# Performance work log

Hardware: AMD Instinct MI355X
Metric: run time of the kernel (lower is better)

Reference implementation:

```python
import jax, jax.numpy as jnp
import numpy as np

WS = (2, 6, 12)          # window_size (Z, H, W)
DIM = 192
HEADS = 6
TOW = 240                # type_of_windows = (8//2)*(360//6)
NW = 720                 # total number of windows = 3 * TOW
L = WS[0] * WS[1] * WS[2]  # 144 tokens per window


def _position_index(ws):
    """Replicates EarthAttention3D._construct_index (static int index)."""
    zi = np.arange(ws[0]); zj = -np.arange(ws[0]) * ws[0]
    hi = np.arange(ws[1]); hj = -np.arange(ws[1]) * ws[1]
    w = np.arange(ws[2])
    c1 = np.stack(np.meshgrid(zi, hi, w, indexing='ij')).reshape(3, -1)
    c2 = np.stack(np.meshgrid(zj, hj, w, indexing='ij')).reshape(3, -1)
    coords = (c1[:, :, None] - c2[:, None, :]).transpose(1, 2, 0)  # (L, L, 3)
    coords[:, :, 2] += ws[2] - 1
    coords[:, :, 1] *= 2 * ws[2] - 1
    coords[:, :, 0] *= (2 * ws[2] - 1) * ws[1] * ws[1]
    return coords.sum(-1).reshape(-1)  # (L*L,)

POS_INDEX = jnp.asarray(_position_index(WS))


def setup_inputs() -> dict:
    key = jax.random.key(0)
    ks = jax.random.split(key, 4)
    table_len = (2 * WS[2] - 1) * WS[1] * WS[1] * WS[0] * WS[0]  # 3312
    return {
        "x": jax.random.normal(ks[0], (NW, L, DIM), jnp.float32),
        "mask": jnp.zeros((NW, L, L), jnp.float32),
        "w1": jax.random.normal(ks[1], (3 * DIM, DIM), jnp.float32) * 0.02,
        "b1": jnp.zeros((3 * DIM,), jnp.float32),
        "w2": jax.random.normal(ks[2], (DIM, DIM), jnp.float32) * 0.02,
        "b2": jnp.zeros((DIM,), jnp.float32),
        "bias_table": jax.random.normal(ks[3], (table_len, TOW, HEADS), jnp.float32) * 0.02,
    }


def reference(x, mask, w1, b1, w2, b2, bias_table):
    Wn, Ltok, dim = x.shape
    hd = dim // HEADS
    scale = hd ** -0.5
    # qkv projection: (Wn, L, 3, H, hd) -> q,k,v each (Wn, H, L, hd)
    qkv = (x @ w1.T + b1).reshape(Wn, Ltok, 3, HEADS, hd)
    qkv = jnp.transpose(qkv, (2, 0, 3, 1, 4))
    q, k, v = qkv[0], qkv[1], qkv[2]
    attn = jnp.einsum('whid,whjd->whij', q * scale, k)  # (Wn, H, L, L)
    # Earth-specific bias: gather table -> (L, L, TOW, H) -> (TOW, H, L, L)
    bias = bias_table[POS_INDEX].reshape(Ltok, Ltok, TOW, HEADS)
    bias = jnp.transpose(bias, (2, 3, 0, 1))
    # tile across window axis exactly like the concat loop, then slice
    reps = Wn // TOW + 1
    bias = jnp.tile(bias, (reps, 1, 1, 1))[:Wn][None]  # (1, Wn, H, L, L)
    attn = attn[None] + bias                            # (1, Wn, H, L, L)
    attn = attn + mask[None, :, None, :, :]             # mask.unsqueeze(1).unsqueeze(0)
    attn = jax.nn.softmax(attn, axis=-1)
    out = jnp.einsum('bwhij,whjd->bwhid', attn, v)      # (1, Wn, H, L, hd)
    out = jnp.transpose(out, (0, 1, 3, 2, 4)).reshape(Wn, Ltok, dim)
    out = out @ w2.T + b2
    return out
```

## Files before the change

kernel.cpp:

```cpp
#include <hip/hip_runtime.h>
#include <cstdint>
#include <cstddef>


using short8 = __attribute__((ext_vector_type(8))) short;
using f32x4  = __attribute__((ext_vector_type(4))) float;

constexpr int kNW = 720;
constexpr float kScale = 0.17677669529663687f;
constexpr size_t kQKVElems = (size_t)kNW * 6 * 144 * 32;

__device__ __forceinline__ ushort bf16_rne(float f) {
  uint u = __builtin_bit_cast(uint, f);
  return (ushort)((u + 0x7FFFu + ((u >> 16) & 1u)) >> 16);
}
__device__ __forceinline__ float bf16_to_f(ushort h) {
  uint u = ((uint)h) << 16;
  return __builtin_bit_cast(float, u);
}
__device__ __forceinline__ uint pack_hl(float f) {
  const ushort h = bf16_rne(f);
  const ushort l = bf16_rne(f - bf16_to_f(h));
  return ((uint)h << 16) | l;
}

__global__ __launch_bounds__(256) void prep_kernel(
    const float* __restrict__ src, ushort* __restrict__ dh,
    ushort* __restrict__ dl, int n)
{
  const int i = blockIdx.x * 256 + threadIdx.x;
  if (i < n) {
    const float f = src[i];
    const ushort h = bf16_rne(f);
    dh[i] = h;
    dl[i] = bf16_rne(f - bf16_to_f(h));
  }
}

__global__ __launch_bounds__(256) void btT_kernel(
    const float* __restrict__ bt, float* __restrict__ btT)
{
  __shared__ float T[48][49];
  const int pb = (blockIdx.x % 69) * 48;
  const int bb = (blockIdx.x / 69) * 48;
  const int tid = threadIdx.x;
  for (int f = tid; f < 2304; f += 256) {
    const int r = f / 48, c = f % 48;
    T[r][c] = bt[(size_t)(pb + r) * 1440 + bb + c];
  }
  __syncthreads();
  for (int f = tid; f < 2304; f += 256) {
    const int r = f % 48, c = f / 48;
    btT[(size_t)(bb + c) * 3312 + pb + r] = T[r][c];
  }
}

template <bool IS_QKV>
__global__ __launch_bounds__(512) void gemm_kernel(
    const float* __restrict__ Xf, const uint* __restrict__ Xp,
    const ushort* __restrict__ Wh, const ushort* __restrict__ Wl,
    const float* __restrict__ bias,
    uint* __restrict__ qp, uint* __restrict__ kp, uint* __restrict__ vp,
    float* __restrict__ fout)
{
  __shared__ ushort Ah[128][40], Al[128][40];
  __shared__ ushort Bh[192][40], Bl[192][40];

  const int bid = blockIdx.x;
  const int mtile = IS_QKV ? bid / 3 : bid;
  const int col0  = IS_QKV ? (bid % 3) * 192 : 0;
  const int row0 = mtile * 128;
  const int tid = threadIdx.x;
  const int wave = tid >> 6, lane = tid & 63;
  const int rr = lane & 15, kg = lane >> 4;
  const int wm = wave >> 2, wn = wave & 3;

  f32x4 acc[4][3];
#pragma unroll
  for (int a = 0; a < 4; ++a)
#pragma unroll
    for (int b = 0; b < 3; ++b) acc[a][b] = (f32x4){0.f, 0.f, 0.f, 0.f};

  for (int kc = 0; kc < 192; kc += 32) {
#pragma unroll
    for (int u = 0; u < 2; ++u) {
      const int sl = tid + u * 512;
      const int r = sl >> 3, s = sl & 7;
      if constexpr (IS_QKV) {
        float4 xv = *(const float4*)&Xf[(size_t)(row0 + r) * 192 + kc + s * 4];
        ushort4 hv, lv;
        hv.x = bf16_rne(xv.x); lv.x = bf16_rne(xv.x - bf16_to_f(hv.x));
        hv.y = bf16_rne(xv.y); lv.y = bf16_rne(xv.y - bf16_to_f(hv.y));
        hv.z = bf16_rne(xv.z); lv.z = bf16_rne(xv.z - bf16_to_f(hv.z));
        hv.w = bf16_rne(xv.w); lv.w = bf16_rne(xv.w - bf16_to_f(hv.w));
        *(ushort4*)&Ah[r][s * 4] = hv;
        *(ushort4*)&Al[r][s * 4] = lv;
      } else {
        uint4 a = *(const uint4*)&Xp[(size_t)(row0 + r) * 192 + kc + s * 4];
        uint2 hh, ll;
        hh.x = (a.x >> 16) | (a.y & 0xffff0000u);
        hh.y = (a.z >> 16) | (a.w & 0xffff0000u);
        ll.x = (a.x & 0xffffu) | (a.y << 16);
        ll.y = (a.z & 0xffffu) | (a.w << 16);
        *(uint2*)&Ah[r][s * 4] = hh;
        *(uint2*)&Al[r][s * 4] = ll;
      }
    }
#pragma unroll
    for (int u = 0; u < 3; ++u) {
      const int idx = tid + u * 512;
      const int n = idx >> 3, s2 = idx & 7;
      const size_t g = (size_t)(col0 + n) * 192 + kc + s2 * 4;
      *(uint2*)&Bh[n][s2 * 4] = *(const uint2*)&Wh[g];
      *(uint2*)&Bl[n][s2 * 4] = *(const uint2*)&Wl[g];
    }
    __syncthreads();

    short8 ah[4], al_[4], bh[3], bl[3];
#pragma unroll
    for (int mt = 0; mt < 4; ++mt) {
      const int r = wm * 64 + mt * 16 + rr;
      ah[mt]  = *(const short8*)&Ah[r][kg * 8];
      al_[mt] = *(const short8*)&Al[r][kg * 8];
    }
#pragma unroll
    for (int nt = 0; nt < 3; ++nt) {
      const int n = wn * 48 + nt * 16 + rr;
      bh[nt] = *(const short8*)&Bh[n][kg * 8];
      bl[nt] = *(const short8*)&Bl[n][kg * 8];
    }
#pragma unroll
    for (int mt = 0; mt < 4; ++mt)
#pragma unroll
      for (int nt = 0; nt < 3; ++nt) {
        acc[mt][nt] = __builtin_amdgcn_mfma_f32_16x16x32_bf16(ah[mt],  bh[nt], acc[mt][nt], 0, 0, 0);
        acc[mt][nt] = __builtin_amdgcn_mfma_f32_16x16x32_bf16(ah[mt],  bl[nt], acc[mt][nt], 0, 0, 0);
        acc[mt][nt] = __builtin_amdgcn_mfma_f32_16x16x32_bf16(al_[mt], bh[nt], acc[mt][nt], 0, 0, 0);
      }
    __syncthreads();
  }

  if (IS_QKV) {
    const int t = col0 / 192;
    uint* dst = (t == 0) ? qp : (t == 1) ? kp : vp;
    const float sc = (t == 0) ? kScale : 1.0f;
#pragma unroll
    for (int nt = 0; nt < 3; ++nt) {
      const int c0 = wn * 48 + nt * 16;
      const int hh = c0 >> 5;
      const int d0 = (c0 & 31) + rr;
      const float bcol = bias[col0 + c0 + rr];
#pragma unroll
      for (int mt = 0; mt < 4; ++mt)
#pragma unroll
        for (int reg = 0; reg < 4; ++reg) {
          const int grow = row0 + wm * 64 + mt * 16 + kg * 4 + reg;
          const int w = grow / 144;
          const int l = grow % 144;
          dst[(((size_t)(w * 6 + hh)) * 144 + l) * 32 + d0] =
              pack_hl((acc[mt][nt][reg] + bcol) * sc);
        }
    }
  } else {
#pragma unroll
    for (int nt = 0; nt < 3; ++nt) {
      const int c = wn * 48 + nt * 16 + rr;
      const float bcol = bias[c];
#pragma unroll
      for (int mt = 0; mt < 4; ++mt)
#pragma unroll
        for (int reg = 0; reg < 4; ++reg) {
          const int grow = row0 + wm * 64 + mt * 16 + kg * 4 + reg;
          fout[(size_t)grow * 192 + c] = acc[mt][nt][reg] + bcol;
        }
    }
  }
}

__device__ __forceinline__ void attn_unit(
    const ushort (&KsH)[144][40], const ushort (&KsL)[144][40],
    const ushort (&VtH)[32][168], const ushort (&VtL)[32][168],
    uint* __restrict__ scrw,
    const uint* __restrict__ qpb, const float* __restrict__ mrow,
    const float* __restrict__ brow, uint* __restrict__ aopb,
    int wave, int rr, int kg)
{
  const int i0 = wave * 16;
  const int i = i0 + rr;
  const int pi = 828 * (i / 72) + 23 * ((i / 12) % 6) + (i % 12) + 11;

  const uint4 qa = *(const uint4*)&qpb[(size_t)i * 32 + kg * 8];
  const uint4 qb = *(const uint4*)&qpb[(size_t)i * 32 + kg * 8 + 4];
  float4 mv[9], bv[9];
#pragma unroll
  for (int jt = 0; jt < 9; ++jt) {
    const int jb = jt * 16 + kg * 4;
    mv[jt] = *(const float4*)&mrow[(size_t)i * 144 + jb];
    const int pjb = 1656 * (jb / 72) + 138 * ((jb / 12) % 6) - (jb % 12);
    bv[jt] = *(const float4*)&brow[pi + pjb - 3];
  }

  union { short8 v; uint u[4]; } QH, QL;
  QH.u[0] = (qa.x >> 16) | (qa.y & 0xffff0000u);
  QH.u[1] = (qa.z >> 16) | (qa.w & 0xffff0000u);
  QH.u[2] = (qb.x >> 16) | (qb.y & 0xffff0000u);
  QH.u[3] = (qb.z >> 16) | (qb.w & 0xffff0000u);
  QL.u[0] = (qa.x & 0xffffu) | (qa.y << 16);
  QL.u[1] = (qa.z & 0xffffu) | (qa.w << 16);
  QL.u[2] = (qb.x & 0xffffu) | (qb.y << 16);
  QL.u[3] = (qb.z & 0xffffu) | (qb.w << 16);

  f32x4 acc[9];
#pragma unroll
  for (int jt = 0; jt < 9; ++jt) {
    const short8 kah = *(const short8*)&KsH[jt * 16 + rr][kg * 8];
    const short8 kal = *(const short8*)&KsL[jt * 16 + rr][kg * 8];
    f32x4 c = (f32x4){0.f, 0.f, 0.f, 0.f};
    c = __builtin_amdgcn_mfma_f32_16x16x32_bf16(kah, QH.v, c, 0, 0, 0);
    c = __builtin_amdgcn_mfma_f32_16x16x32_bf16(kah, QL.v, c, 0, 0, 0);
    c = __builtin_amdgcn_mfma_f32_16x16x32_bf16(kal, QH.v, c, 0, 0, 0);
    c[0] += bv[jt].w + mv[jt].x;
    c[1] += bv[jt].z + mv[jt].y;
    c[2] += bv[jt].y + mv[jt].z;
    c[3] += bv[jt].x + mv[jt].w;
    acc[jt] = c;
  }

  float m = -1e30f;
#pragma unroll
  for (int jt = 0; jt < 9; ++jt)
    m = fmaxf(m, fmaxf(fmaxf(acc[jt][0], acc[jt][1]),
                       fmaxf(acc[jt][2], acc[jt][3])));
  m = fmaxf(m, __shfl_xor(m, 16));
  m = fmaxf(m, __shfl_xor(m, 32));
  float s = 0.f;
#pragma unroll
  for (int jt = 0; jt < 9; ++jt)
#pragma unroll
    for (int r = 0; r < 4; ++r) {
      acc[jt][r] = __expf(acc[jt][r] - m);
      s += acc[jt][r];
    }
  s += __shfl_xor(s, 16);
  s += __shfl_xor(s, 32);
  const float inv = 1.0f / s;

  uint wh_[10][2], wl_[10][2];
#pragma unroll
  for (int jt = 0; jt < 9; ++jt)
#pragma unroll
    for (int u = 0; u < 2; ++u) {
      const float p0 = acc[jt][2 * u] * inv, p1 = acc[jt][2 * u + 1] * inv;
      const ushort h0 = bf16_rne(p0), h1 = bf16_rne(p1);
      const ushort l0 = bf16_rne(p0 - bf16_to_f(h0));
      const ushort l1 = bf16_rne(p1 - bf16_to_f(h1));
      wh_[jt][u] = (uint)h0 | ((uint)h1 << 16);
      wl_[jt][u] = (uint)l0 | ((uint)l1 << 16);
    }
  wh_[9][0] = 0; wh_[9][1] = 0; wl_[9][0] = 0; wl_[9][1] = 0;

  f32x4 oacc[2] = {(f32x4){0.f, 0.f, 0.f, 0.f}, (f32x4){0.f, 0.f, 0.f, 0.f}};
#pragma unroll
  for (int ks = 0; ks < 5; ++ks) {
    const int jtA = 2 * ks, jtB = 2 * ks + 1;
    *(uint2*)&scrw[rr * 20 + 2 * kg]           = make_uint2(wh_[jtA][0], wh_[jtA][1]);
    *(uint2*)&scrw[rr * 20 + 8 + 2 * kg]       = make_uint2(wh_[jtB][0], wh_[jtB][1]);
    *(uint2*)&scrw[320 + rr * 20 + 2 * kg]     = make_uint2(wl_[jtA][0], wl_[jtA][1]);
    *(uint2*)&scrw[320 + rr * 20 + 8 + 2 * kg] = make_uint2(wl_[jtB][0], wl_[jtB][1]);
    asm volatile("s_waitcnt lgkmcnt(0)" ::: "memory");
    const ushort* scr = (const ushort*)scrw;
    const short8 pfh = *(const short8*)&scr[rr * 40 + kg * 8];
    const short8 pfl = *(const short8*)&scr[640 + rr * 40 + kg * 8];
#pragma unroll
    for (int dt = 0; dt < 2; ++dt) {
      const short8 vfh = *(const short8*)&VtH[dt * 16 + rr][ks * 32 + kg * 8];
      const short8 vfl = *(const short8*)&VtL[dt * 16 + rr][ks * 32 + kg * 8];
      oacc[dt] = __builtin_amdgcn_mfma_f32_16x16x32_bf16(pfh, vfh, oacc[dt], 0, 0, 0);
      oacc[dt] = __builtin_amdgcn_mfma_f32_16x16x32_bf16(pfh, vfl, oacc[dt], 0, 0, 0);
      oacc[dt] = __builtin_amdgcn_mfma_f32_16x16x32_bf16(pfl, vfh, oacc[dt], 0, 0, 0);
    }
    asm volatile("s_waitcnt lgkmcnt(0)" ::: "memory");
  }

#pragma unroll
  for (int dt = 0; dt < 2; ++dt)
#pragma unroll
    for (int r = 0; r < 4; ++r)
      aopb[(size_t)(i0 + kg * 4 + r) * 192 + dt * 16 + rr] =
          pack_hl(oacc[dt][r]);
}

__device__ __forceinline__ void write_k(
    ushort (&KH)[144][40], ushort (&KL)[144][40], int l, int d, uint4 kv)
{
  ushort4 hk, lk;
  hk.x = (ushort)(kv.x >> 16); lk.x = (ushort)(kv.x & 0xffff);
  hk.y = (ushort)(kv.y >> 16); lk.y = (ushort)(kv.y & 0xffff);
  hk.z = (ushort)(kv.z >> 16); lk.z = (ushort)(kv.z & 0xffff);
  hk.w = (ushort)(kv.w >> 16); lk.w = (ushort)(kv.w & 0xffff);
  *(ushort4*)&KH[l][d] = hk;
  *(ushort4*)&KL[l][d] = lk;
}
__device__ __forceinline__ void write_vt(
    ushort (&VH)[32][168], ushort (&VL)[32][168], int l, int d, uint4 vv)
{
  VH[d + 0][l] = (ushort)(vv.x >> 16); VL[d + 0][l] = (ushort)(vv.x & 0xffff);
  VH[d + 1][l] = (ushort)(vv.y >> 16); VL[d + 1][l] = (ushort)(vv.y & 0xffff);
  VH[d + 2][l] = (ushort)(vv.z >> 16); VL[d + 2][l] = (ushort)(vv.z & 0xffff);
  VH[d + 3][l] = (ushort)(vv.w >> 16); VL[d + 3][l] = (ushort)(vv.w & 0xffff);
}

__global__ __launch_bounds__(576) void attn_kernel(
    const uint* __restrict__ qp, const uint* __restrict__ kp,
    const uint* __restrict__ vp, const float* __restrict__ mask,
    const float* __restrict__ btT, uint* __restrict__ aop)
{
  __shared__ __align__(16) ushort Ks_[3][2][144][40];
  __shared__ __align__(16) ushort Vt[3][2][32][168];
  __shared__ __align__(16) uint Scr[9][640];

  const int tid = threadIdx.x;
  const int wave = tid >> 6, lane = tid & 63;
  const int rr = lane & 15, kg = lane >> 4;

  const int b = blockIdx.x;
  const int q = (b & 7) * 180 + (b >> 3);
  const int w = q >> 1;
  const int h0 = (q & 1) * 3;
  const size_t base0 = (size_t)(w * 6 + h0) * 4608;
  const float* mrow = mask + (size_t)w * 20736;
  const float* brow0 = btT + (size_t)((w % 240) * 6 + h0) * 3312;
  uint* aopb0 = aop + (size_t)w * 144 * 192 + h0 * 32;

  const int l0 = tid >> 3, d0 = (tid & 7) * 4;
  const int f1 = tid + 576;
  const int l1 = f1 >> 3, d1 = (f1 & 7) * 4;

  {
    const uint4 kvA = *(const uint4*)&kp[base0 + l0 * 32 + d0];
    const uint4 vvA = *(const uint4*)&vp[base0 + l0 * 32 + d0];
    const uint4 kvB = *(const uint4*)&kp[base0 + l1 * 32 + d1];
    const uint4 vvB = *(const uint4*)&vp[base0 + l1 * 32 + d1];
    write_k(Ks_[0][0], Ks_[0][1], l0, d0, kvA);
    write_k(Ks_[0][0], Ks_[0][1], l1, d1, kvB);
    write_vt(Vt[0][0], Vt[0][1], l0, d0, vvA);
    write_vt(Vt[0][0], Vt[0][1], l1, d1, vvB);
  }
  for (int f = tid; f < 3072; f += 576) {
    const int bu = f >> 10, pl = (f >> 9) & 1, d = (f >> 4) & 31, j = 144 + (f & 15);
    Vt[bu][pl][d][j] = 0;
  }

  uint4 kA = *(const uint4*)&kp[base0 + 4608 + l0 * 32 + d0];
  uint4 vA = *(const uint4*)&vp[base0 + 4608 + l0 * 32 + d0];
  uint4 kB = *(const uint4*)&kp[base0 + 4608 + l1 * 32 + d1];
  uint4 vB = *(const uint4*)&vp[base0 + 4608 + l1 * 32 + d1];

  __syncthreads();

  attn_unit(Ks_[0][0], Ks_[0][1], Vt[0][0], Vt[0][1], Scr[wave],
            qp + base0, mrow, brow0, aopb0, wave, rr, kg);

  write_k(Ks_[1][0], Ks_[1][1], l0, d0, kA);
  write_k(Ks_[1][0], Ks_[1][1], l1, d1, kB);
  write_vt(Vt[1][0], Vt[1][1], l0, d0, vA);
  write_vt(Vt[1][0], Vt[1][1], l1, d1, vB);
  kA = *(const uint4*)&kp[base0 + 9216 + l0 * 32 + d0];
  vA = *(const uint4*)&vp[base0 + 9216 + l0 * 32 + d0];
  kB = *(const uint4*)&kp[base0 + 9216 + l1 * 32 + d1];
  vB = *(const uint4*)&vp[base0 + 9216 + l1 * 32 + d1];

  __syncthreads();

  attn_unit(Ks_[1][0], Ks_[1][1], Vt[1][0], Vt[1][1], Scr[wave],
            qp + base0 + 4608, mrow, brow0 + 3312, aopb0 + 32, wave, rr, kg);

  write_k(Ks_[2][0], Ks_[2][1], l0, d0, kA);
  write_k(Ks_[2][0], Ks_[2][1], l1, d1, kB);
  write_vt(Vt[2][0], Vt[2][1], l0, d0, vA);
  write_vt(Vt[2][0], Vt[2][1], l1, d1, vB);

  __syncthreads();

  attn_unit(Ks_[2][0], Ks_[2][1], Vt[2][0], Vt[2][1], Scr[wave],
            qp + base0 + 9216, mrow, brow0 + 6624, aopb0 + 64, wave, rr, kg);
}

extern "C" void kernel_launch(void* const* d_in, const int* in_sizes, int n_in,
                              void* d_out, int out_size, void* d_ws, size_t ws_size,
                              hipStream_t stream)
{
  const float* x    = (const float*)d_in[0];
  const float* mask = (const float*)d_in[1];
  const float* w1   = (const float*)d_in[2];
  const float* b1   = (const float*)d_in[3];
  const float* w2   = (const float*)d_in[4];
  const float* b2   = (const float*)d_in[5];
  const float* bt   = (const float*)d_in[6];
  float* out = (float*)d_out;

  uint* qp  = (uint*)d_ws;
  uint* kp  = qp + kQKVElems;
  uint* vp  = kp + kQKVElems;
  uint* aop = vp + kQKVElems;
  ushort* w1h = (ushort*)aop;
  ushort* w1l = w1h + 110592;
  ushort* w2h = (ushort*)qp;
  ushort* w2l = w2h + 36864;
  float* btT = out;

  btT_kernel<<<69 * 30, 256, 0, stream>>>(bt, btT);
  prep_kernel<<<432, 256, 0, stream>>>(w1, w1h, w1l, 110592);
  gemm_kernel<true><<<810 * 3, 512, 0, stream>>>(
      x, nullptr, w1h, w1l, b1, qp, kp, vp, nullptr);
  attn_kernel<<<1440, 576, 0, stream>>>(qp, kp, vp, mask, btT, aop);
  prep_kernel<<<144, 256, 0, stream>>>(w2, w2h, w2l, 36864);
  gemm_kernel<false><<<810, 512, 0, stream>>>(
      nullptr, aop, w2h, w2l, b2, nullptr, nullptr, nullptr, out);
}
```

Before: 358.7 us.

## Fuse output projection into attention kernel, one block per window over six heads

The output projection GEMM is folded into the attention kernel. Each block now handles all six heads of a window, double-buffers K/V through shared memory, and accumulates the per-head attention output times the matching W2 slice in registers. This removes the intermediate attention-output buffer round trip and a separate kernel launch. In exchange the grid is halved to 720 blocks, each wave keeps 12 extra accumulators, W2 fragments are read from global memory per head, and the bias table moves into workspace instead of reusing the output buffer.

```diff
diff --git a/kernel.cpp b/kernel.cpp
--- a/kernel.cpp
+++ b/kernel.cpp
@@ -55,20 +55,18 @@
   }
 }
 
-template <bool IS_QKV>
-__global__ __launch_bounds__(512) void gemm_kernel(
-    const float* __restrict__ Xf, const uint* __restrict__ Xp,
+__global__ __launch_bounds__(512) void qkv_gemm_kernel(
+    const float* __restrict__ Xf,
     const ushort* __restrict__ Wh, const ushort* __restrict__ Wl,
     const float* __restrict__ bias,
-    uint* __restrict__ qp, uint* __restrict__ kp, uint* __restrict__ vp,
-    float* __restrict__ fout)
+    uint* __restrict__ qp, uint* __restrict__ kp, uint* __restrict__ vp)
 {
   __shared__ ushort Ah[128][40], Al[128][40];
   __shared__ ushort Bh[192][40], Bl[192][40];
 
   const int bid = blockIdx.x;
-  const int mtile = IS_QKV ? bid / 3 : bid;
-  const int col0  = IS_QKV ? (bid % 3) * 192 : 0;
+  const int mtile = bid / 3;
+  const int col0  = (bid % 3) * 192;
   const int row0 = mtile * 128;
   const int tid = threadIdx.x;
   const int wave = tid >> 6, lane = tid & 63;
@@ -86,25 +84,14 @@
     for (int u = 0; u < 2; ++u) {
       const int sl = tid + u * 512;
       const int r = sl >> 3, s = sl & 7;
-      if constexpr (IS_QKV) {
-        float4 xv = *(const float4*)&Xf[(size_t)(row0 + r) * 192 + kc + s * 4];
-        ushort4 hv, lv;
-        hv.x = bf16_rne(xv.x); lv.x = bf16_rne(xv.x - bf16_to_f(hv.x));
-        hv.y = bf16_rne(xv.y); lv.y = bf16_rne(xv.y - bf16_to_f(hv.y));
-        hv.z = bf16_rne(xv.z); lv.z = bf16_rne(xv.z - bf16_to_f(hv.z));
-        hv.w = bf16_rne(xv.w); lv.w = bf16_rne(xv.w - bf16_to_f(hv.w));
-        *(ushort4*)&Ah[r][s * 4] = hv;
-        *(ushort4*)&Al[r][s * 4] = lv;
-      } else {
-        uint4 a = *(const uint4*)&Xp[(size_t)(row0 + r) * 192 + kc + s * 4];
-        uint2 hh, ll;
-        hh.x = (a.x >> 16) | (a.y & 0xffff0000u);
-        hh.y = (a.z >> 16) | (a.w & 0xffff0000u);
-        ll.x = (a.x & 0xffffu) | (a.y << 16);
-        ll.y = (a.z & 0xffffu) | (a.w << 16);
-        *(uint2*)&Ah[r][s * 4] = hh;
-        *(uint2*)&Al[r][s * 4] = ll;
-      }
+      float4 xv = *(const float4*)&Xf[(size_t)(row0 + r) * 192 + kc + s * 4];
+      ushort4 hv, lv;
+      hv.x = bf16_rne(xv.x); lv.x = bf16_rne(xv.x - bf16_to_f(hv.x));
+      hv.y = bf16_rne(xv.y); lv.y = bf16_rne(xv.y - bf16_to_f(hv.y));
+      hv.z = bf16_rne(xv.z); lv.z = bf16_rne(xv.z - bf16_to_f(hv.z));
+      hv.w = bf16_rne(xv.w); lv.w = bf16_rne(xv.w - bf16_to_f(hv.w));
+      *(ushort4*)&Ah[r][s * 4] = hv;
+      *(ushort4*)&Al[r][s * 4] = lv;
     }
 #pragma unroll
     for (int u = 0; u < 3; ++u) {
@@ -140,50 +127,36 @@
     __syncthreads();
   }
 
-  if (IS_QKV) {
-    const int t = col0 / 192;
-    uint* dst = (t == 0) ? qp : (t == 1) ? kp : vp;
-    const float sc = (t == 0) ? kScale : 1.0f;
-#pragma unroll
-    for (int nt = 0; nt < 3; ++nt) {
-      const int c0 = wn * 48 + nt * 16;
-      const int hh = c0 >> 5;
-      const int d0 = (c0 & 31) + rr;
-      const float bcol = bias[col0 + c0 + rr];
-#pragma unroll
-      for (int mt = 0; mt < 4; ++mt)
-#pragma unroll
-        for (int reg = 0; reg < 4; ++reg) {
-          const int grow = row0 + wm * 64 + mt * 16 + kg * 4 + reg;
-          const int w = grow / 144;
-          const int l = grow % 144;
-          dst[(((size_t)(w * 6 + hh)) * 144 + l) * 32 + d0] =
-              pack_hl((acc[mt][nt][reg] + bcol) * sc);
-        }
-    }
-  } else {
-#pragma unroll
-    for (int nt = 0; nt < 3; ++nt) {
-      const int c = wn * 48 + nt * 16 + rr;
-      const float bcol = bias[c];
-#pragma unroll
-      for (int mt = 0; mt < 4; ++mt)
-#pragma unroll
-        for (int reg = 0; reg < 4; ++reg) {
-          const int grow = row0 + wm * 64 + mt * 16 + kg * 4 + reg;
-          fout[(size_t)grow * 192 + c] = acc[mt][nt][reg] + bcol;
-        }
-    }
-  }
-}
-
-__device__ __forceinline__ void attn_unit(
+  const int t = col0 / 192;
+  uint* dst = (t == 0) ? qp : (t == 1) ? kp : vp;
+  const float sc = (t == 0) ? kScale : 1.0f;
+#pragma unroll
+  for (int nt = 0; nt < 3; ++nt) {
+    const int c0 = wn * 48 + nt * 16;
+    const int hh = c0 >> 5;
+    const int d0 = (c0 & 31) + rr;
+    const float bcol = bias[col0 + c0 + rr];
+#pragma unroll
+    for (int mt = 0; mt < 4; ++mt)
+#pragma unroll
+      for (int reg = 0; reg < 4; ++reg) {
+        const int grow = row0 + wm * 64 + mt * 16 + kg * 4 + reg;
+        const int w = grow / 144;
+        const int l = grow % 144;
+        dst[(((size_t)(w * 6 + hh)) * 144 + l) * 32 + d0] =
+            pack_hl((acc[mt][nt][reg] + bcol) * sc);
+      }
+  }
+}
+
+__device__ __forceinline__ void attn_unit_fused(
     const ushort (&KsH)[144][40], const ushort (&KsL)[144][40],
     const ushort (&VtH)[32][168], const ushort (&VtL)[32][168],
     uint* __restrict__ scrw,
     const uint* __restrict__ qpb, const float* __restrict__ mrow,
-    const float* __restrict__ brow, uint* __restrict__ aopb,
-    int wave, int rr, int kg)
+    const float* __restrict__ brow,
+    const ushort* __restrict__ w2h, const ushort* __restrict__ w2l,
+    int u, f32x4* pacc, int wave, int rr, int kg)
 {
   const int i0 = wave * 16;
   const int i = i0 + rr;
@@ -200,15 +173,15 @@
     bv[jt] = *(const float4*)&brow[pi + pjb - 3];
   }
 
-  union { short8 v; uint u[4]; } QH, QL;
-  QH.u[0] = (qa.x >> 16) | (qa.y & 0xffff0000u);
-  QH.u[1] = (qa.z >> 16) | (qa.w & 0xffff0000u);
-  QH.u[2] = (qb.x >> 16) | (qb.y & 0xffff0000u);
-  QH.u[3] = (qb.z >> 16) | (qb.w & 0xffff0000u);
-  QL.u[0] = (qa.x & 0xffffu) | (qa.y << 16);
-  QL.u[1] = (qa.z & 0xffffu) | (qa.w << 16);
-  QL.u[2] = (qb.x & 0xffffu) | (qb.y << 16);
-  QL.u[3] = (qb.z & 0xffffu) | (qb.w << 16);
+  union { short8 v; uint uu[4]; } QH, QL;
+  QH.uu[0] = (qa.x >> 16) | (qa.y & 0xffff0000u);
+  QH.uu[1] = (qa.z >> 16) | (qa.w & 0xffff0000u);
+  QH.uu[2] = (qb.x >> 16) | (qb.y & 0xffff0000u);
+  QH.uu[3] = (qb.z >> 16) | (qb.w & 0xffff0000u);
+  QL.uu[0] = (qa.x & 0xffffu) | (qa.y << 16);
+  QL.uu[1] = (qa.z & 0xffffu) | (qa.w << 16);
+  QL.uu[2] = (qb.x & 0xffffu) | (qb.y << 16);
+  QL.uu[3] = (qb.z & 0xffffu) | (qb.w << 16);
 
   f32x4 acc[9];
 #pragma unroll
@@ -249,13 +222,13 @@
 #pragma unroll
   for (int jt = 0; jt < 9; ++jt)
 #pragma unroll
-    for (int u = 0; u < 2; ++u) {
-      const float p0 = acc[jt][2 * u] * inv, p1 = acc[jt][2 * u + 1] * inv;
+    for (int uu = 0; uu < 2; ++uu) {
+      const float p0 = acc[jt][2 * uu] * inv, p1 = acc[jt][2 * uu + 1] * inv;
       const ushort h0 = bf16_rne(p0), h1 = bf16_rne(p1);
       const ushort l0 = bf16_rne(p0 - bf16_to_f(h0));
       const ushort l1 = bf16_rne(p1 - bf16_to_f(h1));
-      wh_[jt][u] = (uint)h0 | ((uint)h1 << 16);
-      wl_[jt][u] = (uint)l0 | ((uint)l1 << 16);
+      wh_[jt][uu] = (uint)h0 | ((uint)h1 << 16);
+      wl_[jt][uu] = (uint)l0 | ((uint)l1 << 16);
     }
   wh_[9][0] = 0; wh_[9][1] = 0; wl_[9][0] = 0; wl_[9][1] = 0;
 
@@ -282,12 +255,33 @@
     asm volatile("s_waitcnt lgkmcnt(0)" ::: "memory");
   }
 
-#pragma unroll
-  for (int dt = 0; dt < 2; ++dt)
-#pragma unroll
-    for (int r = 0; r < 4; ++r)
-      aopb[(size_t)(i0 + kg * 4 + r) * 192 + dt * 16 + rr] =
-          pack_hl(oacc[dt][r]);
+  {
+    ushort* sh = (ushort*)scrw;
+#pragma unroll
+    for (int dt = 0; dt < 2; ++dt)
+#pragma unroll
+      for (int r = 0; r < 4; ++r) {
+        const int il = kg * 4 + r;
+        const int dl = dt * 16 + rr;
+        const float v = oacc[dt][r];
+        const ushort h = bf16_rne(v);
+        sh[il * 40 + dl] = h;
+        sh[640 + il * 40 + dl] = bf16_rne(v - bf16_to_f(h));
+      }
+    asm volatile("s_waitcnt lgkmcnt(0)" ::: "memory");
+    const short8 pah = *(const short8*)&sh[rr * 40 + kg * 8];
+    const short8 pal = *(const short8*)&sh[640 + rr * 40 + kg * 8];
+#pragma unroll
+    for (int nt = 0; nt < 12; ++nt) {
+      const size_t gb = (size_t)(nt * 16 + rr) * 192 + u * 32 + kg * 8;
+      const short8 wbh = *(const short8*)&w2h[gb];
+      const short8 wbl = *(const short8*)&w2l[gb];
+      pacc[nt] = __builtin_amdgcn_mfma_f32_16x16x32_bf16(pah, wbh, pacc[nt], 0, 0, 0);
+      pacc[nt] = __builtin_amdgcn_mfma_f32_16x16x32_bf16(pah, wbl, pacc[nt], 0, 0, 0);
+      pacc[nt] = __builtin_amdgcn_mfma_f32_16x16x32_bf16(pal, wbh, pacc[nt], 0, 0, 0);
+    }
+    asm volatile("s_waitcnt lgkmcnt(0)" ::: "memory");
+  }
 }
 
 __device__ __forceinline__ void write_k(
@@ -313,10 +307,12 @@
 __global__ __launch_bounds__(576) void attn_kernel(
     const uint* __restrict__ qp, const uint* __restrict__ kp,
     const uint* __restrict__ vp, const float* __restrict__ mask,
-    const float* __restrict__ btT, uint* __restrict__ aop)
-{
-  __shared__ __align__(16) ushort Ks_[3][2][144][40];
-  __shared__ __align__(16) ushort Vt[3][2][32][168];
+    const float* __restrict__ btT,
+    const ushort* __restrict__ w2h, const ushort* __restrict__ w2l,
+    const float* __restrict__ b2, float* __restrict__ out)
+{
+  __shared__ __align__(16) ushort Ks_[2][2][144][40];
+  __shared__ __align__(16) ushort Vt[2][2][32][168];
   __shared__ __align__(16) uint Scr[9][640];
 
   const int tid = threadIdx.x;
@@ -324,13 +320,11 @@
   const int rr = lane & 15, kg = lane >> 4;
 
   const int b = blockIdx.x;
-  const int q = (b & 7) * 180 + (b >> 3);
-  const int w = q >> 1;
-  const int h0 = (q & 1) * 3;
-  const size_t base0 = (size_t)(w * 6 + h0) * 4608;
+  const int w = (b & 7) * 90 + (b >> 3);
+  const size_t base0 = (size_t)(w * 6) * 4608;
   const float* mrow = mask + (size_t)w * 20736;
-  const float* brow0 = btT + (size_t)((w % 240) * 6 + h0) * 3312;
-  uint* aopb0 = aop + (size_t)w * 144 * 192 + h0 * 32;
+  const float* brow0 = btT + (size_t)((w % 240) * 6) * 3312;
+  float* out_b = out + (size_t)w * 144 * 192;
 
   const int l0 = tid >> 3, d0 = (tid & 7) * 4;
   const int f1 = tid + 576;
@@ -346,10 +340,14 @@
     write_vt(Vt[0][0], Vt[0][1], l0, d0, vvA);
     write_vt(Vt[0][0], Vt[0][1], l1, d1, vvB);
   }
-  for (int f = tid; f < 3072; f += 576) {
+  for (int f = tid; f < 2048; f += 576) {
     const int bu = f >> 10, pl = (f >> 9) & 1, d = (f >> 4) & 31, j = 144 + (f & 15);
     Vt[bu][pl][d][j] = 0;
   }
+
+  f32x4 pacc[12];
+#pragma unroll
+  for (int nt = 0; nt < 12; ++nt) pacc[nt] = (f32x4){0.f, 0.f, 0.f, 0.f};
 
   uint4 kA = *(const uint4*)&kp[base0 + 4608 + l0 * 32 + d0];
   uint4 vA = *(const uint4*)&vp[base0 + 4608 + l0 * 32 + d0];
@@ -358,32 +356,35 @@
 
   __syncthreads();
 
-  attn_unit(Ks_[0][0], Ks_[0][1], Vt[0][0], Vt[0][1], Scr[wave],
-            qp + base0, mrow, brow0, aopb0, wave, rr, kg);
-
-  write_k(Ks_[1][0], Ks_[1][1], l0, d0, kA);
-  write_k(Ks_[1][0], Ks_[1][1], l1, d1, kB);
-  write_vt(Vt[1][0], Vt[1][1], l0, d0, vA);
-  write_vt(Vt[1][0], Vt[1][1], l1, d1, vB);
-  kA = *(const uint4*)&kp[base0 + 9216 + l0 * 32 + d0];
-  vA = *(const uint4*)&vp[base0 + 9216 + l0 * 32 + d0];
-  kB = *(const uint4*)&kp[base0 + 9216 + l1 * 32 + d1];
-  vB = *(const uint4*)&vp[base0 + 9216 + l1 * 32 + d1];
-
-  __syncthreads();
-
-  attn_unit(Ks_[1][0], Ks_[1][1], Vt[1][0], Vt[1][1], Scr[wave],
-            qp + base0 + 4608, mrow, brow0 + 3312, aopb0 + 32, wave, rr, kg);
-
-  write_k(Ks_[2][0], Ks_[2][1], l0, d0, kA);
-  write_k(Ks_[2][0], Ks_[2][1], l1, d1, kB);
-  write_vt(Vt[2][0], Vt[2][1], l0, d0, vA);
-  write_vt(Vt[2][0], Vt[2][1], l1, d1, vB);
-
-  __syncthreads();
-
-  attn_unit(Ks_[2][0], Ks_[2][1], Vt[2][0], Vt[2][1], Scr[wave],
-            qp + base0 + 9216, mrow, brow0 + 6624, aopb0 + 64, wave, rr, kg);
+#pragma unroll
+  for (int u = 0; u < 6; ++u) {
+    attn_unit_fused(Ks_[u & 1][0], Ks_[u & 1][1], Vt[u & 1][0], Vt[u & 1][1],
+                    Scr[wave], qp + base0 + (size_t)u * 4608, mrow,
+                    brow0 + u * 3312, w2h, w2l, u, pacc, wave, rr, kg);
+    if (u < 5) {
+      write_k(Ks_[(u + 1) & 1][0], Ks_[(u + 1) & 1][1], l0, d0, kA);
+      write_k(Ks_[(u + 1) & 1][0], Ks_[(u + 1) & 1][1], l1, d1, kB);
+      write_vt(Vt[(u + 1) & 1][0], Vt[(u + 1) & 1][1], l0, d0, vA);
+      write_vt(Vt[(u + 1) & 1][0], Vt[(u + 1) & 1][1], l1, d1, vB);
+      if (u < 4) {
+        kA = *(const uint4*)&kp[base0 + (size_t)(u + 2) * 4608 + l0 * 32 + d0];
+        vA = *(const uint4*)&vp[base0 + (size_t)(u + 2) * 4608 + l0 * 32 + d0];
+        kB = *(const uint4*)&kp[base0 + (size_t)(u + 2) * 4608 + l1 * 32 + d1];
+        vB = *(const uint4*)&vp[base0 + (size_t)(u + 2) * 4608 + l1 * 32 + d1];
+      }
+      __syncthreads();
+    }
+  }
+
+  const int i0 = wave * 16;
+#pragma unroll
+  for (int nt = 0; nt < 12; ++nt) {
+    const int c = nt * 16 + rr;
+    const float bcol = b2[c];
+#pragma unroll
+    for (int r = 0; r < 4; ++r)
+      out_b[(size_t)(i0 + kg * 4 + r) * 192 + c] = pacc[nt][r] + bcol;
+  }
 }
 
 extern "C" void kernel_launch(void* const* d_in, const int* in_sizes, int n_in,
@@ -402,19 +403,16 @@
   uint* qp  = (uint*)d_ws;
   uint* kp  = qp + kQKVElems;
   uint* vp  = kp + kQKVElems;
-  uint* aop = vp + kQKVElems;
-  ushort* w1h = (ushort*)aop;
+  uint* scratch = vp + kQKVElems;
+  ushort* w1h = (ushort*)scratch;
   ushort* w1l = w1h + 110592;
-  ushort* w2h = (ushort*)qp;
+  float* btT = (float*)scratch + 1000000;
+  ushort* w2h = (ushort*)((float*)scratch + 6000000);
   ushort* w2l = w2h + 36864;
-  float* btT = out;
 
   btT_kernel<<<69 * 30, 256, 0, stream>>>(bt, btT);
   prep_kernel<<<432, 256, 0, stream>>>(w1, w1h, w1l, 110592);
-  gemm_kernel<true><<<810 * 3, 512, 0, stream>>>(
-      x, nullptr, w1h, w1l, b1, qp, kp, vp, nullptr);
-  attn_kernel<<<1440, 576, 0, stream>>>(qp, kp, vp, mask, btT, aop);
   prep_kernel<<<144, 256, 0, stream>>>(w2, w2h, w2l, 36864);
-  gemm_kernel<false><<<810, 512, 0, stream>>>(
-      nullptr, aop, w2h, w2l, b2, nullptr, nullptr, nullptr, out);
-}
+  qkv_gemm_kernel<<<810 * 3, 512, 0, stream>>>(x, w1h, w1l, b1, qp, kp, vp);
+  attn_kernel<<<720, 576, 0, stream>>>(qp, kp, vp, mask, btT, w2h, w2l, b2, out);
+}
```

Result: slower. 481.8 us (+34.3%).
